# Kernel optimization log

Measured on AMD Instinct MI355X. Metric: run time of the kernel, lower is better.

The kernel has to match this reference:

```python
import jax, jax.numpy as jnp
import numpy as np

B, T, C = 2, 2048, 1024
H = 16
HS = C // H  # 64

def setup_inputs() -> dict:
    key = jax.random.key(0)
    ks = jax.random.split(key, 5)
    s = 0.02  # typical init scale for stability
    return {
        "x": jax.random.normal(ks[0], (B, T, C), dtype=jnp.float32),
        "Wq": jax.random.normal(ks[1], (C, C), dtype=jnp.float32) * s,
        "Wk": jax.random.normal(ks[2], (C, C), dtype=jnp.float32) * s,
        "Wv": jax.random.normal(ks[3], (C, C), dtype=jnp.float32) * s,
        "Wp": jax.random.normal(ks[4], (C, C), dtype=jnp.float32) * s,
    }

def reference(x, Wq, Wk, Wv, Wp):
    b, t, c = x.shape
    # nn.Linear(bias=False): y = x @ W.T
    q = (x @ Wq.T).reshape(b, t, H, HS).transpose(0, 2, 1, 3)  # [b,h,t,hs]
    k = (x @ Wk.T).reshape(b, t, H, HS).transpose(0, 2, 1, 3)
    v = (x @ Wv.T).reshape(b, t, H, HS).transpose(0, 2, 1, 3)
    att = jnp.einsum('bhqd,bhkd->bhqk', q, k) / jnp.sqrt(jnp.float32(HS))
    # quirk: masked_fill with 0 (NOT -inf) on the strict upper triangle, then softmax
    mask = jnp.triu(jnp.ones((t, t), dtype=bool), k=1)
    att = jnp.where(mask, 0.0, att)
    att = jax.nn.softmax(att, axis=-1)
    y = jnp.einsum('bhqk,bhkd->bhqd', att, v)  # [b,h,t,hs]
    y = y.transpose(0, 2, 1, 3).reshape(b, t, c)
    return y @ Wp.T
```

## Files before the change

kernel.cpp:

```cpp
#include <hip/hip_runtime.h>
#include <hip/hip_bf16.h>
#include <math.h>

#define BB 2
#define TT 2048
#define CC 1024
#define HH 16
#define HS 64
#define NROWS (BB * TT)
#define QTILES (TT / 64)

typedef __attribute__((ext_vector_type(8))) short short8v;
typedef __attribute__((ext_vector_type(4))) float f32x4;
typedef __attribute__((ext_vector_type(4))) unsigned int u32x4;
typedef unsigned short u16;

__device__ __forceinline__ u16 f2bf(float f) {
    return __builtin_bit_cast(u16, (__bf16)f);
}

__device__ __forceinline__ void glds16(const void* g, void* l) {
    __builtin_amdgcn_global_load_lds((__attribute__((address_space(1))) void*)g,
                                     (__attribute__((address_space(3))) void*)l, 16, 0, 0);
}
#define WAITV(N) asm volatile("s_waitcnt vmcnt(" #N ")" ::: "memory")
#define BAR() do { __builtin_amdgcn_s_barrier(); __builtin_amdgcn_sched_barrier(0); } while (0)

__device__ __forceinline__ void swap32(unsigned& a, unsigned& b) {
    asm volatile("v_permlane32_swap_b32 %0, %1" : "+v"(a), "+v"(b));
}
__device__ __forceinline__ void swap16(unsigned& a, unsigned& b) {
    asm volatile("v_permlane16_swap_b32 %0, %1" : "+v"(a), "+v"(b));
}

__global__ __launch_bounds__(256) void fsplit_kernel(const float* __restrict__ x,
                                                     const float* __restrict__ Wq, const float* __restrict__ Wk,
                                                     const float* __restrict__ Wv, const float* __restrict__ Wp,
                                                     u16* __restrict__ xh,
                                                     u16* __restrict__ wqk,
                                                     u16* __restrict__ wv, u16* __restrict__ wp) {
    const size_t WC = (size_t)CC * CC;
    const int bid = blockIdx.x;
    const float* src; u16* dh; float sc = 1.f; int i;
    if (bid < 4096) {
        src = x; dh = xh; i = bid * 256 + threadIdx.x;
    } else {
        const int wsel = (bid - 4096) >> 10;
        i = ((bid - 4096) & 1023) * 256 + threadIdx.x;
        if (wsel == 0)      { src = Wq; dh = wqk;      sc = 0.125f * 1.4426950408889634f; }
        else if (wsel == 1) { src = Wk; dh = wqk + WC; }
        else if (wsel == 2) { src = Wv; dh = wv; }
        else                { src = Wp; dh = wp; }
    }
    float4 v = ((const float4*)src)[i];
    v.x *= sc; v.y *= sc; v.z *= sc; v.w *= sc;
    ushort4 H;
    H.x = f2bf(v.x); H.y = f2bf(v.y); H.z = f2bf(v.z); H.w = f2bf(v.w);
    ((ushort4*)dh)[i] = H;
}

__global__ __launch_bounds__(256) void qkv_kernel(const u16* __restrict__ xh, const u16* __restrict__ wqk,
                                                  const u16* __restrict__ wv,
                                                  u16* __restrict__ Qo, u16* __restrict__ Ko,
                                                  u16* __restrict__ VtO, float* __restrict__ TSg) {
    __shared__ u16 lA[2 * 4096], lB[2 * 4096];
    const int tid = threadIdx.x;
    const int lane = tid & 63, w = tid >> 6;
    const int wr = w >> 1, wc = w & 1;
    const int fr = lane & 15, fc = lane >> 4;
    const int K = CC;

    const int gbid = blockIdx.x;
    const bool isQK = gbid < 512;
    const int sub = isQK ? gbid : gbid - 512;
    const int nbx = isQK ? 16 : 32;
    const int nwg = isQK ? 512 : 256;
    const u16* __restrict__ A = isQK ? xh : wv;
    const u16* __restrict__ B = isQK ? wqk : xh;

    const int swz = (sub & 7) * (nwg >> 3) + (sub >> 3);
    const int bm = (swz / nbx) * 128, bn = (swz % nbx) * 128;

    f32x4 acc[4][4];
    #pragma unroll
    for (int i = 0; i < 4; ++i)
        #pragma unroll
        for (int j = 0; j < 4; ++j) acc[i][j] = (f32x4){0.f, 0.f, 0.f, 0.f};

    const int lrow = lane >> 2, lcs = lane & 3;
    const int rA0 = w * 16 + lrow, rA1 = rA0 + 64;
    const size_t aoff0 = (size_t)(bm + rA0) * K + (lcs ^ ((rA0 >> 1) & 3)) * 8;
    const size_t aoff1 = (size_t)(bm + rA1) * K + (lcs ^ ((rA1 >> 1) & 3)) * 8;
    const size_t boff0 = (size_t)(bn + rA0) * K + (lcs ^ ((rA0 >> 1) & 3)) * 8;
    const size_t boff1 = (size_t)(bn + rA1) * K + (lcs ^ ((rA1 >> 1) & 3)) * 8;
    const int d0 = w * 512, d1 = 2048 + w * 512;

    int aslot[4], bslot[4];
    #pragma unroll
    for (int mi = 0; mi < 4; ++mi) {
        int row = wr * 64 + mi * 16 + fr;
        aslot[mi] = row * 4 + (fc ^ ((row >> 1) & 3));
    }
    #pragma unroll
    for (int ni = 0; ni < 4; ++ni) {
        int col = wc * 64 + ni * 16 + fr;
        bslot[ni] = col * 4 + (fc ^ ((col >> 1) & 3));
    }

    auto STAGE = [&](int t, int buf) {
        const int k0 = t * 32;
        const int bo = buf * 4096;
        glds16(A + aoff0 + k0, lA + bo + d0);
        glds16(A + aoff1 + k0, lA + bo + d1);
        glds16(B + boff0 + k0, lB + bo + d0);
        glds16(B + boff1 + k0, lB + bo + d1);
    };

    const int nt = K >> 5;
    STAGE(0, 0);

    #pragma unroll 2
    for (int t = 0; t < nt; ++t) {
        const int cur = t & 1;
        BAR();
        if (t + 1 < nt) { STAGE(t + 1, cur ^ 1); WAITV(4); }
        else            { WAITV(0); }

        const int co = cur * 512;
        short8v fa[4], fb[4];
        #pragma unroll
        for (int mi = 0; mi < 4; ++mi) fa[mi] = ((const short8v*)lA)[co + aslot[mi]];
        #pragma unroll
        for (int ni = 0; ni < 4; ++ni) fb[ni] = ((const short8v*)lB)[co + bslot[ni]];
        __builtin_amdgcn_s_setprio(1);
        #pragma unroll
        for (int mi = 0; mi < 4; ++mi)
            #pragma unroll
            for (int ni = 0; ni < 4; ++ni)
                acc[mi][ni] = __builtin_amdgcn_mfma_f32_16x16x32_bf16(fa[mi], fb[ni], acc[mi][ni], 0, 0, 0);
        __builtin_amdgcn_s_setprio(0);
    }

    const int fq = lane >> 4;
    if (isQK) {
        #pragma unroll
        for (int mi = 0; mi < 4; ++mi)
            #pragma unroll
            for (int ni = 0; ni < 4; ++ni)
                #pragma unroll
                for (int r = 0; r < 4; ++r) {
                    const int rg = bm + wr * 64 + mi * 16 + fq * 4 + r;
                    const int cg = bn + wc * 64 + ni * 16 + fr;
                    const u16 hh = f2bf(acc[mi][ni][r]);
                    if (cg < CC) Qo[(size_t)rg * CC + cg] = hh;
                    else         Ko[(size_t)rg * CC + cg - CC] = hh;
                }
    } else {
        #pragma unroll
        for (int mi = 0; mi < 4; ++mi)
            #pragma unroll
            for (int ni = 0; ni < 4; ++ni)
                #pragma unroll
                for (int r = 0; r < 4; ++r) {
                    const int rg = bm + wr * 64 + mi * 16 + fq * 4 + r;
                    const int cg = bn + wc * 64 + ni * 16 + fr;
                    const int bq = cg >> 11, tq = cg & 2047;
                    const int hq = rg >> 6, dq = rg & 63;
                    VtO[((size_t)((bq << 4) + hq) * HS + dq) * TT + tq] = f2bf(acc[mi][ni][r]);
                }
        __syncthreads();
        float* TSL = (float*)lA;
        #pragma unroll
        for (int mi = 0; mi < 4; ++mi)
            #pragma unroll
            for (int r = 0; r < 4; ++r) {
                float s = acc[mi][0][r] + acc[mi][1][r] + acc[mi][2][r] + acc[mi][3][r];
                s += __shfl_xor(s, 1); s += __shfl_xor(s, 2);
                s += __shfl_xor(s, 4); s += __shfl_xor(s, 8);
                if (fr == 0) TSL[wc * 128 + wr * 64 + mi * 16 + fq * 4 + r] = s;
            }
        __syncthreads();
        {
            const int wcq = tid >> 7, row = tid & 127;
            const int col0 = bn + wcq * 64;
            const int bq = col0 >> 11, qtv = (col0 & 2047) >> 6;
            const int bhh = (bq << 4) + ((bm + row) >> 6);
            const int dq = (bm + row) & 63;
            TSg[((size_t)bhh * QTILES + qtv) * 64 + dq] = TSL[tid];
        }
    }
}

__global__ __launch_bounds__(256) void gemm_proj(const u16* __restrict__ A, const u16* __restrict__ B,
                                                 float* __restrict__ O, int M, int N, int K) {
    __shared__ u16 lA[2 * 4096], lB[2 * 4096];
    const int tid = threadIdx.x;
    const int lane = tid & 63, w = tid >> 6;
    const int wr = w >> 1, wc = w & 1;
    const int fr = lane & 15, fc = lane >> 4;

    const int nbx = gridDim.x;
    const int bid = blockIdx.y * nbx + blockIdx.x;
    const int nwg = nbx * gridDim.y;
    const int swz = (bid & 7) * (nwg >> 3) + (bid >> 3);
    const int bm = (swz / nbx) * 128, bn = (swz % nbx) * 128;

    f32x4 acc[4][4];
    #pragma unroll
    for (int i = 0; i < 4; ++i)
        #pragma unroll
        for (int j = 0; j < 4; ++j) acc[i][j] = (f32x4){0.f, 0.f, 0.f, 0.f};

    const int lrow = lane >> 2, lcs = lane & 3;
    const int rA0 = w * 16 + lrow, rA1 = rA0 + 64;
    const size_t aoff0 = (size_t)(bm + rA0) * K + (lcs ^ ((rA0 >> 1) & 3)) * 8;
    const size_t aoff1 = (size_t)(bm + rA1) * K + (lcs ^ ((rA1 >> 1) & 3)) * 8;
    const size_t boff0 = (size_t)(bn + rA0) * K + (lcs ^ ((rA0 >> 1) & 3)) * 8;
    const size_t boff1 = (size_t)(bn + rA1) * K + (lcs ^ ((rA1 >> 1) & 3)) * 8;
    const int d0 = w * 512, d1 = 2048 + w * 512;

    int aslot[4], bslot[4];
    #pragma unroll
    for (int mi = 0; mi < 4; ++mi) {
        int row = wr * 64 + mi * 16 + fr;
        aslot[mi] = row * 4 + (fc ^ ((row >> 1) & 3));
    }
    #pragma unroll
    for (int ni = 0; ni < 4; ++ni) {
        int col = wc * 64 + ni * 16 + fr;
        bslot[ni] = col * 4 + (fc ^ ((col >> 1) & 3));
    }

    auto STAGE = [&](int t, int buf) {
        const int k0 = t * 32;
        const int bo = buf * 4096;
        glds16(A + aoff0 + k0, lA + bo + d0);
        glds16(A + aoff1 + k0, lA + bo + d1);
        glds16(B + boff0 + k0, lB + bo + d0);
        glds16(B + boff1 + k0, lB + bo + d1);
    };

    const int nt = K >> 5;
    STAGE(0, 0);

    #pragma unroll 2
    for (int t = 0; t < nt; ++t) {
        const int cur = t & 1;
        BAR();
        if (t + 1 < nt) { STAGE(t + 1, cur ^ 1); WAITV(4); }
        else            { WAITV(0); }

        const int co = cur * 512;
        short8v fa[4], fb[4];
        #pragma unroll
        for (int mi = 0; mi < 4; ++mi) fa[mi] = ((const short8v*)lA)[co + aslot[mi]];
        #pragma unroll
        for (int ni = 0; ni < 4; ++ni) fb[ni] = ((const short8v*)lB)[co + bslot[ni]];
        __builtin_amdgcn_s_setprio(1);
        #pragma unroll
        for (int mi = 0; mi < 4; ++mi)
            #pragma unroll
            for (int ni = 0; ni < 4; ++ni)
                acc[mi][ni] = __builtin_amdgcn_mfma_f32_16x16x32_bf16(fa[mi], fb[ni], acc[mi][ni], 0, 0, 0);
        __builtin_amdgcn_s_setprio(0);
    }

    const int fq = lane >> 4;
    #pragma unroll
    for (int mi = 0; mi < 4; ++mi)
        #pragma unroll
        for (int ni = 0; ni < 4; ++ni)
            #pragma unroll
            for (int r = 0; r < 4; ++r) {
                const int rg = bm + wr * 64 + mi * 16 + fq * 4 + r;
                const int cg = bn + wc * 64 + ni * 16 + fr;
                O[(size_t)rg * N + cg] = acc[mi][ni][r];
            }
}

__global__ __launch_bounds__(256, 4) void attn_kernel(const u16* __restrict__ Qh,
                                                      const u16* __restrict__ Kh,
                                                      const u16* __restrict__ Vt,
                                                      const float* __restrict__ TSg,
                                                      u16* __restrict__ Yh) {
    const int g = blockIdx.x;
    const int bh = (g & 7) + 8 * ((g >> 3) & 3);
    const int qt = 31 - (g >> 5);
    const int b = bh >> 4, h = bh & 15;
    const int tid = threadIdx.x;
    const int w = tid >> 6, lane = tid & 63;
    const int lx = lane & 15, hi4 = lane >> 4;

    __shared__ u16 Ksh[2 * 4096];
    __shared__ u16 Vsh[2 * 4096];
    __shared__ float stp4[4][64];
    __shared__ float stS[64];

    const u16* Kg = Kh + (size_t)b * TT * CC + h * HS;
    const u16* Vg = Vt + (size_t)bh * HS * TT;

    const int s0 = w * 64 + lane, s1 = 256 + w * 64 + lane;
    const int rr0 = s0 >> 3, gc0 = (s0 & 7) ^ (rr0 & 7);
    const int rr1 = s1 >> 3, gc1 = (s1 & 7) ^ (rr1 & 7);
    const int db0 = (w * 64) * 8, db1 = (256 + w * 64) * 8;
    const size_t kbase0 = (size_t)rr0 * CC + gc0 * 8;
    const size_t kbase1 = (size_t)rr1 * CC + gc1 * 8;
    const size_t vbase0 = (size_t)rr0 * TT + gc0 * 8;
    const size_t vbase1 = (size_t)rr1 * TT + gc1 * 8;

    auto stage = [&](int kt, int buf) {
        const size_t ko = (size_t)kt * 64 * CC;
        const int vo = kt * 64;
        const int bo = buf * 4096;
        glds16(Kg + ko + kbase0, Ksh + bo + db0);
        glds16(Kg + ko + kbase1, Ksh + bo + db1);
        glds16(Vg + vbase0 + vo, Vsh + bo + db0);
        glds16(Vg + vbase1 + vo, Vsh + bo + db1);
    };

    stage(0, 0);

    {
        const int d = tid & 63, grp = tid >> 6;
        float part = 0.f;
        for (int t2 = qt + grp; t2 < QTILES; t2 += 4)
            part += TSg[((size_t)bh * QTILES + t2) * 64 + d];
        stp4[grp][d] = part;
        __syncthreads();
        if (tid < 64) stS[tid] = stp4[0][tid] + stp4[1][tid] + stp4[2][tid] + stp4[3][tid];
        __syncthreads();
    }

    short8v nones[2];
    #pragma unroll
    for (int k0 = 0; k0 < 2; ++k0)
        #pragma unroll
        for (int jj = 0; jj < 8; ++jj)
            nones[k0][jj] = (short)(((k0 * 32 + hi4 * 8 + jj) <= (w * 16 + lx)) ? 0xBF80 : 0);

    const size_t qoff = (size_t)(b * TT + qt * 64 + w * 16 + lx) * CC + h * HS + hi4 * 8;
    short8v qf[2];
    qf[0] = *(const short8v*)(Qh + qoff); qf[1] = *(const short8v*)(Qh + qoff + 32);

    const f32x4 zero = {0.f, 0.f, 0.f, 0.f};
    f32x4 y4[4];
    float lsum = 0.f;
    #pragma unroll
    for (int dt = 0; dt < 4; ++dt) y4[dt] = zero;

    int cur = 0;
    for (int kt = 0; kt <= qt; ++kt) {
        WAITV(0);
        BAR();
        if (kt < qt) stage(kt + 1, cur ^ 1);

        const int co = cur * 512;
        const bool diag = (kt == qt);

        f32x4 s4[4];
        #pragma unroll
        for (int j = 0; j < 4; ++j) s4[j] = zero;
        __builtin_amdgcn_s_setprio(1);
        #pragma unroll
        for (int j = 0; j < 4; ++j) {
            const int keyr = j * 16 + lx;
            const int rb = keyr * 8, sw = keyr & 7;
            #pragma unroll
            for (int d0 = 0; d0 < 2; ++d0) {
                const short8v kb = ((const short8v*)Ksh)[co + rb + ((hi4 + 4 * d0) ^ sw)];
                s4[j] = __builtin_amdgcn_mfma_f32_16x16x32_bf16(kb, qf[d0], s4[j], 0, 0, 0);
            }
        }
        __builtin_amdgcn_s_setprio(0);

        unsigned Wpk[4][2];
        #pragma unroll
        for (int j = 0; j < 4; ++j) {
            float pv[4];
            #pragma unroll
            for (int r = 0; r < 4; ++r) {
                float e = __builtin_amdgcn_exp2f(s4[j][r]);
                if (diag && (j * 16 + hi4 * 4 + r) > (w * 16 + lx)) e = 0.f;
                lsum += e;
                pv[r] = e;
            }
            Wpk[j][0] = (unsigned)f2bf(pv[0]) | ((unsigned)f2bf(pv[1]) << 16);
            Wpk[j][1] = (unsigned)f2bf(pv[2]) | ((unsigned)f2bf(pv[3]) << 16);
        }
        #pragma unroll
        for (int j1 = 0; j1 < 2; ++j1)
            #pragma unroll
            for (int hh = 0; hh < 2; ++hh) {
                swap32(Wpk[2 * j1][hh], Wpk[2 * j1 + 1][hh]);
                swap16(Wpk[2 * j1][hh], Wpk[2 * j1 + 1][hh]);
            }
        short8v pa[2];
        #pragma unroll
        for (int k0 = 0; k0 < 2; ++k0) {
            u32x4 ah = {Wpk[2 * k0][0], Wpk[2 * k0][1], Wpk[2 * k0 + 1][0], Wpk[2 * k0 + 1][1]};
            pa[k0] = __builtin_bit_cast(short8v, ah);
        }

        __builtin_amdgcn_s_setprio(1);
        #pragma unroll
        for (int dt = 0; dt < 4; ++dt) {
            const int drow = dt * 16 + lx;
            const int rb = drow * 8, sw = drow & 7;
            #pragma unroll
            for (int k0 = 0; k0 < 2; ++k0) {
                const short8v vb = ((const short8v*)Vsh)[co + rb + ((hi4 + 4 * k0) ^ sw)];
                y4[dt] = __builtin_amdgcn_mfma_f32_16x16x32_bf16(pa[k0], vb, y4[dt], 0, 0, 0);
                if (diag)
                    y4[dt] = __builtin_amdgcn_mfma_f32_16x16x32_bf16(nones[k0], vb, y4[dt], 0, 0, 0);
            }
        }
        __builtin_amdgcn_s_setprio(0);

        cur ^= 1;
    }

    lsum += __shfl_xor(lsum, 16);
    lsum += __shfl_xor(lsum, 32);
    float l4[4];
    #pragma unroll
    for (int r = 0; r < 4; ++r) l4[r] = __shfl(lsum, hi4 * 4 + r);

    #pragma unroll
    for (int dt = 0; dt < 4; ++dt) {
        const float st = stS[dt * 16 + lx];
        #pragma unroll
        for (int r = 0; r < 4; ++r) {
            const int t = qt * 64 + w * 16 + hi4 * 4 + r;
            const float linv = 1.f / (l4[r] + (float)(TT - 1 - t));
            const float yv = (y4[dt][r] + st) * linv;
            const size_t off = (size_t)(b * TT + t) * CC + h * HS + dt * 16 + lx;
            Yh[off] = f2bf(yv);
        }
    }
}

extern "C" void kernel_launch(void* const* d_in, const int* in_sizes, int n_in,
                              void* d_out, int out_size, void* d_ws, size_t ws_size,
                              hipStream_t stream) {
    const float* x  = (const float*)d_in[0];
    const float* Wq = (const float*)d_in[1];
    const float* Wk = (const float*)d_in[2];
    const float* Wv = (const float*)d_in[3];
    const float* Wp = (const float*)d_in[4];
    float* out = (float*)d_out;

    char* ws = (char*)d_ws;
    u16* xh = (u16*)ws;
    u16* Yh = xh;
    u16* Qh = (u16*)(ws + (16u << 20));
    u16* Kh = (u16*)(ws + (32u << 20));
    u16* wv = (u16*)(ws + (48u << 20));
    float* TSg = (float*)(ws + (52u << 20));
    u16* wp = (u16*)(ws + (56u << 20));
    u16* wqk = (u16*)out;
    u16* Vth = (u16*)((char*)out + (4u << 20));

    fsplit_kernel<<<8192, 256, 0, stream>>>(x, Wq, Wk, Wv, Wp, xh, wqk, wv, wp);

    qkv_kernel<<<768, 256, 0, stream>>>(xh, wqk, wv, Qh, Kh, Vth, TSg);

    attn_kernel<<<1024, 256, 0, stream>>>(Qh, Kh, Vth, TSg, Yh);

    gemm_proj<<<dim3(CC / 128, NROWS / 128), 256, 0, stream>>>(Yh, wp, out, NROWS, CC, CC);
}
```

Before: 104.9 us.

## Pair complementary causal query tiles per attention block for load balance

Each attention block now handles two query tiles, qt=31-p and qt=p, running their key loops back to back in one pipelined loop, so every block does the same total of 33 key tiles. The grid is halved from 1024 to 512 blocks. This is meant to remove the tail imbalance of causal attention, where some blocks do 32 tiles and others do 1. In exchange there is less parallelism, extra register pressure from holding both Q fragments, and a per-iteration select between them.

```diff
diff --git a/kernel.cpp b/kernel.cpp
--- a/kernel.cpp
+++ b/kernel.cpp
@@ -285,7 +285,8 @@
                                                       u16* __restrict__ Yh) {
     const int g = blockIdx.x;
     const int bh = (g & 7) + 8 * ((g >> 3) & 3);
-    const int qt = 31 - (g >> 5);
+    const int p = g >> 5;
+    const int qta = 31 - p, qtb = p;
     const int b = bh >> 4, h = bh & 15;
     const int tid = threadIdx.x;
     const int w = tid >> 6, lane = tid & 63;
@@ -293,8 +294,8 @@
 
     __shared__ u16 Ksh[2 * 4096];
     __shared__ u16 Vsh[2 * 4096];
-    __shared__ float stp4[4][64];
-    __shared__ float stS[64];
+    __shared__ float stp4[2][4][64];
+    __shared__ float stS[2][64];
 
     const u16* Kg = Kh + (size_t)b * TT * CC + h * HS;
     const u16* Vg = Vt + (size_t)bh * HS * TT;
@@ -322,12 +323,19 @@
 
     {
         const int d = tid & 63, grp = tid >> 6;
-        float part = 0.f;
-        for (int t2 = qt + grp; t2 < QTILES; t2 += 4)
-            part += TSg[((size_t)bh * QTILES + t2) * 64 + d];
-        stp4[grp][d] = part;
+        float pA = 0.f, pB = 0.f;
+        for (int t2 = qtb + grp; t2 < QTILES; t2 += 4) {
+            const float v = TSg[((size_t)bh * QTILES + t2) * 64 + d];
+            pB += v;
+            if (t2 >= qta) pA += v;
+        }
+        stp4[0][grp][d] = pA;
+        stp4[1][grp][d] = pB;
         __syncthreads();
-        if (tid < 64) stS[tid] = stp4[0][tid] + stp4[1][tid] + stp4[2][tid] + stp4[3][tid];
+        if (tid < 128) {
+            const int hf = tid >> 6, dd = tid & 63;
+            stS[hf][dd] = stp4[hf][0][dd] + stp4[hf][1][dd] + stp4[hf][2][dd] + stp4[hf][3][dd];
+        }
         __syncthreads();
     }
 
@@ -338,9 +346,11 @@
         for (int jj = 0; jj < 8; ++jj)
             nones[k0][jj] = (short)(((k0 * 32 + hi4 * 8 + jj) <= (w * 16 + lx)) ? 0xBF80 : 0);
 
-    const size_t qoff = (size_t)(b * TT + qt * 64 + w * 16 + lx) * CC + h * HS + hi4 * 8;
-    short8v qf[2];
-    qf[0] = *(const short8v*)(Qh + qoff); qf[1] = *(const short8v*)(Qh + qoff + 32);
+    const size_t qoffA = (size_t)(b * TT + qta * 64 + w * 16 + lx) * CC + h * HS + hi4 * 8;
+    const size_t qoffB = (size_t)(b * TT + qtb * 64 + w * 16 + lx) * CC + h * HS + hi4 * 8;
+    short8v qfA[2], qfB[2];
+    qfA[0] = *(const short8v*)(Qh + qoffA); qfA[1] = *(const short8v*)(Qh + qoffA + 32);
+    qfB[0] = *(const short8v*)(Qh + qoffB); qfB[1] = *(const short8v*)(Qh + qoffB + 32);
 
     const f32x4 zero = {0.f, 0.f, 0.f, 0.f};
     f32x4 y4[4];
@@ -348,11 +358,21 @@
     #pragma unroll
     for (int dt = 0; dt < 4; ++dt) y4[dt] = zero;
 
+    const int unitsA = qta + 1;
+    const int total = unitsA + qtb + 1;
+    int qt = qta;
+    int hf = 0;
     int cur = 0;
-    for (int kt = 0; kt <= qt; ++kt) {
+    for (int u = 0; u < total; ++u) {
+        const int kt = (u >= unitsA) ? (u - unitsA) : u;
+
         WAITV(0);
         BAR();
-        if (kt < qt) stage(kt + 1, cur ^ 1);
+        if (u + 1 < total) {
+            const int nu = u + 1;
+            const int nkt = (nu >= unitsA) ? (nu - unitsA) : nu;
+            stage(nkt, cur ^ 1);
+        }
 
         const int co = cur * 512;
         const bool diag = (kt == qt);
@@ -368,7 +388,8 @@
             #pragma unroll
             for (int d0 = 0; d0 < 2; ++d0) {
                 const short8v kb = ((const short8v*)Ksh)[co + rb + ((hi4 + 4 * d0) ^ sw)];
-                s4[j] = __builtin_amdgcn_mfma_f32_16x16x32_bf16(kb, qf[d0], s4[j], 0, 0, 0);
+                const short8v qv = hf ? qfB[d0] : qfA[d0];
+                s4[j] = __builtin_amdgcn_mfma_f32_16x16x32_bf16(kb, qv, s4[j], 0, 0, 0);
             }
         }
         __builtin_amdgcn_s_setprio(0);
@@ -416,26 +437,34 @@
         }
         __builtin_amdgcn_s_setprio(0);
 
+        if (diag) {
+            float ls = lsum;
+            ls += __shfl_xor(ls, 16);
+            ls += __shfl_xor(ls, 32);
+            float l4[4];
+            #pragma unroll
+            for (int r = 0; r < 4; ++r) l4[r] = __shfl(ls, hi4 * 4 + r);
+
+            #pragma unroll
+            for (int dt = 0; dt < 4; ++dt) {
+                const float st = stS[hf][dt * 16 + lx];
+                #pragma unroll
+                for (int r = 0; r < 4; ++r) {
+                    const int t = qt * 64 + w * 16 + hi4 * 4 + r;
+                    const float linv = 1.f / (l4[r] + (float)(TT - 1 - t));
+                    const float yv = (y4[dt][r] + st) * linv;
+                    const size_t off = (size_t)(b * TT + t) * CC + h * HS + dt * 16 + lx;
+                    Yh[off] = f2bf(yv);
+                }
+            }
+            #pragma unroll
+            for (int dt = 0; dt < 4; ++dt) y4[dt] = zero;
+            lsum = 0.f;
+            qt = qtb;
+            hf = 1;
+        }
+
         cur ^= 1;
-    }
-
-    lsum += __shfl_xor(lsum, 16);
-    lsum += __shfl_xor(lsum, 32);
-    float l4[4];
-    #pragma unroll
-    for (int r = 0; r < 4; ++r) l4[r] = __shfl(lsum, hi4 * 4 + r);
-
-    #pragma unroll
-    for (int dt = 0; dt < 4; ++dt) {
-        const float st = stS[dt * 16 + lx];
-        #pragma unroll
-        for (int r = 0; r < 4; ++r) {
-            const int t = qt * 64 + w * 16 + hi4 * 4 + r;
-            const float linv = 1.f / (l4[r] + (float)(TT - 1 - t));
-            const float yv = (y4[dt][r] + st) * linv;
-            const size_t off = (size_t)(b * TT + t) * CC + h * HS + dt * 16 + lx;
-            Yh[off] = f2bf(yv);
-        }
     }
 }
 
@@ -464,7 +493,7 @@
 
     qkv_kernel<<<768, 256, 0, stream>>>(xh, wqk, wv, Qh, Kh, Vth, TSg);
 
-    attn_kernel<<<1024, 256, 0, stream>>>(Qh, Kh, Vth, TSg, Yh);
+    attn_kernel<<<512, 256, 0, stream>>>(Qh, Kh, Vth, TSg, Yh);
 
     gemm_proj<<<dim3(CC / 128, NROWS / 128), 256, 0, stream>>>(Yh, wp, out, NROWS, CC, CC);
 }
```

After: 115.2 us. +9.8%, slower.
